# Kernel tuning notes

Measured on AMD Instinct MI355X. Metric: run time of the kernel, lower is better.

The kernel has to match this reference:

```python
import jax, jax.numpy as jnp
import numpy as np
from math import comb

N_DERIV = 4          # num_derivatives
ODE_DIM = 512        # ode_dimension
K = ODE_DIM * (N_DERIV + 1)


def _build_system(n, d):
    # system_matrices_1d: A_1d = flip(pascal), Q_1d = flip(hilbert), chol(Q_1d)
    x = np.arange(n + 1)
    B = np.array([[comb(i, j) for j in range(n + 1)] for i in range(n + 1)], dtype=np.float64)
    A1 = B[::-1, ::-1]                                  # flip both axes
    Hil = 1.0 / (x[:, None] + x[None, :] + 1.0)
    Q1 = Hil[::-1, ::-1]
    L1 = np.linalg.cholesky(Q1)
    a = np.kron(np.eye(d), A1)
    q = np.kron(np.eye(d), L1)
    return jnp.asarray(a, jnp.float32), jnp.asarray(q, jnp.float32)


def _qr_r(x):
    # sqrtm_to_cholesky: upper-triangular factor from reduced QR
    return jnp.linalg.qr(x)[1]


def setup_inputs() -> dict:
    key = jax.random.key(0)
    k1, k2, k3, k4, k5 = jax.random.split(key, 5)
    a, q_sqrtm_lower = _build_system(N_DERIV, ODE_DIM)
    m0 = jax.random.normal(k1, (K,), dtype=jnp.float32)
    l0 = jnp.tril(jax.random.normal(k2, (K, K), dtype=jnp.float32) * 0.05)
    H = jax.random.normal(k3, (ODE_DIM, K), dtype=jnp.float32) * 0.1
    bias = jax.random.normal(k4, (ODE_DIM,), dtype=jnp.float32)
    dt = jax.random.uniform(k5, (1,), dtype=jnp.float32, minval=0.05, maxval=0.15)
    return {"m0": m0, "l0": l0, "H": H, "bias": bias, "dt": dt,
            "a": a, "q_sqrtm_lower": q_sqrtm_lower}


def reference(m0, l0, H, bias, dt, a, q_sqrtm_lower):
    d = H.shape[0]
    k = m0.shape[0]
    n1 = k // d                       # num_derivatives + 1
    # --- assemble_preconditioner ---
    powers = jnp.arange(n1 - 1, -1, -1, dtype=m0.dtype)
    scales = jnp.exp(jax.lax.lgamma(powers + 1.0))
    pw = powers + 0.5
    adt = jnp.abs(dt[0])
    p = jnp.tile(adt ** pw / scales, d)          # (k,)
    p_inv = jnp.tile(adt ** (-pw) * scales, d)   # (k,)
    # --- extrapolate_mean ---
    m0_p = p_inv * m0
    m_ext_p = a @ m0_p
    m_ext = p * m_ext_p
    # EK-style linearized observation residual
    m_obs = H @ m_ext - bias                     # (d,)
    # --- estimate_error ---
    l_obs_ns_e = H @ (p_inv[:, None] * q_sqrtm_lower)            # (d,k)
    l_obs_raw = _qr_r(l_obs_ns_e.T).T                            # lower (d,d)
    res_white = jax.scipy.linalg.solve_triangular(l_obs_raw.T, m_obs, lower=False)
    diffusion = jnp.sqrt(jnp.dot(res_white, res_white) / res_white.size)
    error = diffusion * jnp.sqrt(jnp.einsum('nj,nj->n', l_obs_raw, l_obs_raw))
    # --- complete_extrapolation (sum_of_sqrtm_factors) ---
    R1 = (a @ (p_inv[:, None] * l0)).T           # (k,k)
    R2 = (diffusion * q_sqrtm_lower).T           # (k,k)
    l_ext_p = _qr_r(jnp.vstack([R1, R2])).T      # lower (k,k)
    l_ext = p[:, None] * l_ext_p
    # --- final_correction ---
    l_obs_ns = H @ l_ext                         # (d,k)
    l_obs = _qr_r(l_obs_ns.T).T                  # lower (d,d)
    crosscov = l_ext @ l_obs_ns.T                # (k,d)
    gain = jax.scipy.linalg.cho_solve((l_obs, True), crosscov.T).T  # (k,d)
    m_cor = m_ext - gain @ m_obs
    l_cor = l_ext - gain @ l_obs_ns
    u = jnp.reshape(m_cor, (-1, d), order='F')[0]  # derivative-0 block
    return m_cor, l_cor, u, error, diffusion
```

## Files before the change

### kernel.cpp

```cpp
#include <hip/hip_runtime.h>
#include <math.h>

#define KDIM 2560
#define DDIM 512
#define NB 64

#define QM 2560
#define QM2 1024
#define QN 512
#define PW 16
#define UW 4

#define OUT_LCOR 2560
#define OUT_U    6556160
#define OUT_ERR  6556672
#define OUT_DIFF 6557184


__global__ void k_setup(const float* dt, double* scal){
  if (threadIdx.x==0 && blockIdx.x==0){
    double adt = fabs((double)dt[0]);
    const double scales[5] = {24.0,6.0,2.0,1.0,1.0};
    for (int i=0;i<5;i++){
      double pw = (double)(4-i)+0.5;
      scal[i]   = pow(adt, pw)/scales[i];
      scal[5+i] = pow(adt,-pw)*scales[i];
    }
  }
}

__global__ __launch_bounds__(256) void k_mext_mobs(const float* a, const float* m0, const float* H,
                                                   const float* bias, const double* scal,
                                                   double* mext, double* mobs){
  __shared__ double me[KDIM];
  __shared__ double red[256];
  double pp[5], pv[5];
  #pragma unroll
  for (int i=0;i<5;i++){ pp[i]=scal[i]; pv[i]=scal[5+i]; }
  int tid=threadIdx.x;
  for (int r=tid; r<KDIM; r+=256){
    int j=r/5, i=r%5;
    const float* arow = a + (size_t)r*KDIM + 5*j;
    const float* m0b  = m0 + 5*j;
    double acc=0;
    #pragma unroll
    for (int l=0;l<5;l++) acc += (double)arow[l]*pv[l]*(double)m0b[l];
    me[r] = pp[i]*acc;
  }
  __syncthreads();
  if (blockIdx.x==0) for (int r=tid;r<KDIM;r+=256) mext[r]=me[r];
  int b = blockIdx.x;
  const float* Hr = H + (size_t)b*KDIM;
  double acc=0;
  for (int c=tid;c<KDIM;c+=256) acc += (double)Hr[c]*me[c];
  red[tid]=acc; __syncthreads();
  for (int s=128;s>0;s>>=1){ if (tid<s) red[tid]+=red[tid+s]; __syncthreads(); }
  if (tid==0) mobs[b] = red[0] - (double)bias[b];
}

__global__ void k_A2(const float* H, const float* q, const double* scal,
                     double* Atop, double* Abot){
  int idx = blockIdx.x*blockDim.x+threadIdx.x;
  if (idx >= QN*QM) return;
  double pv[5];
  #pragma unroll
  for (int t=0;t<5;t++) pv[t]=scal[5+t];
  int j = idx / QM;
  int i = idx % QM;
  int bi = i/5;
  double acc=0;
  #pragma unroll
  for (int t=0;t<5;t++)
    acc += (double)H[(size_t)j*QM + 5*bi+t]*pv[t]*(double)q[(size_t)(5*bi+t)*QM + i];
  if (i < 512) Atop[(size_t)j*QM2 + i] = acc;
  else         Abot[(size_t)j*2048 + (i-512)] = acc;
}

__global__ void k_copyB(const double* Gbot, double* AQ){
  int idx = blockIdx.x*blockDim.x+threadIdx.x;
  if (idx >= 512*512) return;
  int c = idx/512, rr = idx%512;
  AQ[(size_t)c*QM2 + 512 + rr] = (rr<=c) ? Gbot[(size_t)c*512 + rr] : 0.0;
}

__global__ __launch_bounds__(1024) void qr_panel(double* A, double* vhead, int col0, double* Tbuf){
  __shared__ double redw[16][PW];
  __shared__ double rednorm[16];
  __shared__ double sh[3];
  __shared__ double wsh[PW];
  __shared__ double alphas[PW], betas[PW];
  __shared__ double VtVs[PW][PW];
  __shared__ double Tsh[PW][PW];
  int tid=threadIdx.x, wid=tid>>6, lane=tid&63;
  int m = QM2 - col0;
  bool on = tid < m;
  double x[PW];
  #pragma unroll
  for (int j=0;j<PW;j++)
    x[j] = on ? A[(size_t)(col0+j)*QM2 + col0 + tid] : 0.0;
  for (int j=0;j<PW;j++){
    double v0 = (tid>=j && on)? x[j] : 0.0;
    double ps = v0*v0;
    #pragma unroll
    for (int o=32;o>0;o>>=1) ps += __shfl_down(ps,o);
    if (lane==0) rednorm[wid]=ps;
    if (tid==j) sh[0]=x[j];
    __syncthreads();
    if (tid==0){
      double s0=0;
      for (int t=0;t<16;t++) s0+=rednorm[t];
      double x1=sh[0];
      double nrm=sqrt(s0);
      double alpha=(x1>=0.0)?-nrm:nrm;
      double v1=x1-alpha;
      double vtv=s0-2.0*alpha*x1+alpha*alpha;
      double b=(vtv>0.0)?2.0/vtv:0.0;
      sh[1]=v1; sh[2]=b;
      alphas[j]=alpha; betas[j]=b;
      vhead[col0+j]=v1;
    }
    __syncthreads();
    if (tid==j) x[j]=sh[1];
    double b=sh[2];
    double v=(tid>=j && on)? x[j] : 0.0;
    #pragma unroll
    for (int t=0;t<PW;t++){
      if (t==j) continue;
      double p=v*x[t];
      #pragma unroll
      for (int o=32;o>0;o>>=1) p+=__shfl_down(p,o);
      if (lane==0) redw[wid][t]=p;
    }
    __syncthreads();
    if (tid<PW && tid!=j){
      double tot=0;
      #pragma unroll
      for (int t2=0;t2<16;t2++) tot+=redw[t2][tid];
      if (tid>j) wsh[tid]=b*tot;
      else       VtVs[tid][j]=tot;
    }
    __syncthreads();
    if (v!=0.0){
      for (int t=j+1;t<PW;t++) x[t]-=wsh[t]*v;
    }
  }
  __syncthreads();
  if (tid<PW){
    int i=tid;
    Tsh[i][i]=betas[i];
    for (int j2=i+1;j2<PW;j2++){
      double z=0;
      for (int t=i;t<j2;t++) z+=Tsh[i][t]*VtVs[t][j2];
      Tsh[i][j2]=-betas[j2]*z;
    }
  }
  __syncthreads();
  for (int e=tid;e<PW*PW;e+=1024){
    int i=e/PW, j2=e%PW;
    Tbuf[e] = (j2>=i)? Tsh[i][j2] : 0.0;
  }
  if (on){
    #pragma unroll
    for (int j=0;j<PW;j++)
      A[(size_t)(col0+j)*QM2 + col0 + tid] = (tid==j)? alphas[j] : x[j];
  }
}

__global__ __launch_bounds__(256) void qr_update(double* A, const double* vhead,
                                                 const double* Tbuf, int col0){
  __shared__ double redu[4][PW];
  __shared__ double ysh[PW];
  __shared__ double wsh[PW];
  int tid=threadIdx.x, wid=tid>>6, lane=tid&63;
  int cc=col0+PW+blockIdx.x;
  int m=QM2-col0;
  double a[UW];
  #pragma unroll
  for (int w=0;w<UW;w++){
    int lr=tid+w*256;
    a[w]=(lr<m)? A[(size_t)cc*QM2+col0+lr] : 0.0;
  }
  double acc[PW];
  #pragma unroll
  for (int j=0;j<PW;j++) acc[j]=0;
  #pragma unroll
  for (int w=0;w<UW;w++){
    int lr=tid+w*256;
    if (lr<m){
      #pragma unroll
      for (int j=0;j<PW;j++){
        double vj;
        if (lr>j)       vj=A[(size_t)(col0+j)*QM2+col0+lr];
        else if (lr==j) vj=vhead[col0+j];
        else            vj=0.0;
        acc[j]+=vj*a[w];
      }
    }
  }
  #pragma unroll
  for (int j=0;j<PW;j++){
    double d=acc[j];
    #pragma unroll
    for (int o=32;o>0;o>>=1) d+=__shfl_down(d,o);
    if (lane==0) redu[wid][j]=d;
  }
  __syncthreads();
  if (tid<PW){
    double y=0;
    #pragma unroll
    for (int t=0;t<4;t++) y+=redu[t][tid];
    ysh[tid]=y;
  }
  __syncthreads();
  if (tid<PW){
    double s=0;
    for (int t=0;t<=tid;t++) s+=Tbuf[t*PW+tid]*ysh[t];
    wsh[tid]=s;
  }
  __syncthreads();
  #pragma unroll
  for (int w=0;w<UW;w++){
    int lr=tid+w*256;
    if (lr<m){
      double s=0;
      #pragma unroll
      for (int j=0;j<PW;j++){
        double vj;
        if (lr>j)       vj=A[(size_t)(col0+j)*QM2+col0+lr];
        else if (lr==j) vj=vhead[col0+j];
        else            vj=0.0;
        s+=vj*wsh[j];
      }
      A[(size_t)cc*QM2+col0+lr]=a[w]-s;
    }
  }
}

__global__ __launch_bounds__(512) void k_rpost(const double* Aq, const double* mobs,
                                               double* scal, float* out){
  __shared__ double b[DDIM];
  __shared__ double xs[DDIM];
  __shared__ double D[NB][NB+1];
  __shared__ double red[DDIM];
  __shared__ double g1sh[DDIM];
  int tid=threadIdx.x;
  {
    double s=0;
    for (int r=0;r<=tid;r++){ double v=Aq[(size_t)tid*QM2 + r]; s+=v*v; }
    g1sh[tid]=s;
  }
  b[tid]=mobs[tid];
  __syncthreads();
  for (int p=7;p>=0;p--){
    int b0=p*NB;
    for (int e=tid;e<NB*NB;e+=512){ int i=e&63, j2=e>>6; D[i][j2]=Aq[(size_t)(b0+j2)*QM2 + b0+i]; }
    __syncthreads();
    if (tid<64){
      double bi=b[b0+tid];
      for (int k=NB-1;k>=0;k--){
        double bk=__shfl(bi,k);
        double xk=bk/D[k][k];
        if (tid<k) bi-=D[tid][k]*xk;
        if (tid==k) bi=xk;
      }
      xs[b0+tid]=bi;
    }
    __syncthreads();
    if (tid<b0){
      double s=0;
      #pragma unroll 8
      for (int j2=0;j2<NB;j2++) s+=Aq[(size_t)(b0+j2)*QM2 + tid]*xs[b0+j2];
      b[tid]-=s;
    }
    __syncthreads();
  }
  red[tid]=xs[tid]*xs[tid]; __syncthreads();
  for (int s=256;s>0;s>>=1){ if (tid<s) red[tid]+=red[tid+s]; __syncthreads(); }
  double diff=sqrt(red[0]/(double)DDIM);
  if (tid==0){ scal[10]=diff; out[OUT_DIFF]=(float)diff; }
  out[OUT_ERR+tid]=(float)(diff*sqrt(fmax(g1sh[tid],0.0)));
}

__global__ void k_X(const float* a, const float* l0, const double* scal, float* X){
  int idx=blockIdx.x*blockDim.x+threadIdx.x;
  if (idx>=KDIM*KDIM) return;
  double pv[5];
  #pragma unroll
  for (int t=0;t<5;t++) pv[t]=scal[5+t];
  int r=idx/KDIM, c=idx%KDIM;
  int j=r/5;
  const float* arow = a + (size_t)r*KDIM + 5*j;
  double acc=0;
  #pragma unroll
  for (int l=0;l<5;l++)
    acc += (double)arow[l]*pv[l]*(double)l0[(size_t)(5*j+l)*KDIM+c];
  X[idx]=(float)acc;
}

template<typename TA,int ATR,typename TB,int BTR,int MODE>
__global__ __launch_bounds__(256) void gemm64(const TA* __restrict__ A,int lda,
                                              const TB* __restrict__ B,int ldb,
                                              void* __restrict__ Cv,int ldc,
                                              int K,int kmode){
  __shared__ double As[16][65];
  __shared__ double Bs[16][65];
  int tid=threadIdx.x, tx=tid&15, ty=tid>>4;
  int n0=blockIdx.x*64, m0=blockIdx.y*64;
  int ks=0, ke=K;
  if (kmode==1) ks=n0;
  else if (kmode==2) ke=min(K,n0+64);
  else if (kmode==3) ke=min(K,m0+64);
  else if (kmode==4) ks=m0;
  double acc[4][4]={};
  for (int k0=ks;k0<ke;k0+=16){
    if (ATR){
      for (int e=tid;e<16*64;e+=256){int k=e>>6,mm=e&63; As[k][mm]=(double)A[(size_t)(k0+k)*lda+m0+mm];}
    } else {
      for (int e=tid;e<64*16;e+=256){int mm=e>>4,k=e&15; As[k][mm]=(double)A[(size_t)(m0+mm)*lda+k0+k];}
    }
    if (BTR){
      for (int e=tid;e<64*16;e+=256){int nn=e>>4,k=e&15; Bs[k][nn]=(double)B[(size_t)(n0+nn)*ldb+k0+k];}
    } else {
      for (int e=tid;e<16*64;e+=256){int k=e>>6,nn=e&63; Bs[k][nn]=(double)B[(size_t)(k0+k)*ldb+n0+nn];}
    }
    __syncthreads();
    #pragma unroll
    for (int t=0;t<16;t++){
      double av[4],bv[4];
      #pragma unroll
      for (int i=0;i<4;i++){av[i]=As[t][ty+16*i];bv[i]=Bs[t][tx+16*i];}
      #pragma unroll
      for (int i=0;i<4;i++)
        #pragma unroll
        for (int j=0;j<4;j++) acc[i][j]+=av[i]*bv[j];
    }
    __syncthreads();
  }
  #pragma unroll
  for (int i=0;i<4;i++){
    #pragma unroll
    for (int j=0;j<4;j++){
      size_t idx=(size_t)(m0+ty+16*i)*ldc+n0+tx+16*j;
      if (MODE==0) ((double*)Cv)[idx]=acc[i][j];
      else if (MODE==1) ((double*)Cv)[idx]-=acc[i][j];
      else ((float*)Cv)[idx]=(float)acc[i][j];
    }
  }
}

__global__ __launch_bounds__(256) void syrk_lower(const float* __restrict__ X, const float* __restrict__ q,
                                                  const double* __restrict__ scal,
                                                  double* __restrict__ G, int n){
  int S0=blockIdx.x*64, R0=blockIdx.y*64;
  if (S0>R0) return;
  __shared__ double As[16][65];
  __shared__ double Bs[16][65];
  int tid=threadIdx.x, tx=tid&15, ty=tid>>4;
  int kend=min(n, S0+80);
  double acc[4][4]={};
  for (int k0=0;k0<kend;k0+=16){
    for (int e=tid;e<64*16;e+=256){int mm=e>>4,k=e&15; As[k][mm]=(double)X[(size_t)(R0+mm)*n+k0+k];}
    for (int e=tid;e<64*16;e+=256){int nn=e>>4,k=e&15; Bs[k][nn]=(double)X[(size_t)(S0+nn)*n+k0+k];}
    __syncthreads();
    #pragma unroll
    for (int t=0;t<16;t++){
      double av[4],bv[4];
      #pragma unroll
      for (int i=0;i<4;i++){av[i]=As[t][ty+16*i];bv[i]=Bs[t][tx+16*i];}
      #pragma unroll
      for (int i=0;i<4;i++)
        #pragma unroll
        for (int j=0;j<4;j++) acc[i][j]+=av[i]*bv[j];
    }
    __syncthreads();
  }
  double dd = scal[10]*scal[10];
  #pragma unroll
  for (int i=0;i<4;i++)
    #pragma unroll
    for (int j=0;j<4;j++){
      int r=R0+ty+16*i, c=S0+tx+16*j;
      double v=acc[i][j];
      if (c<=r && (r/5)==(c/5)){
        double qq=0;
        #pragma unroll
        for (int k=0;k<5;k++) qq += (double)q[(size_t)(r%5)*KDIM+k]*(double)q[(size_t)(c%5)*KDIM+k];
        v += dd*qq;
      }
      G[(size_t)r*n+c]=v;
    }
}

__global__ __launch_bounds__(256) void chol_diag(double* A, int n, int k0){
  __shared__ double P[NB][NB+1];
  int tid=threadIdx.x;
  for (int e=tid;e<NB*NB;e+=256){int r=e>>6,c=e&63;P[r][c]=A[(size_t)(k0+r)*n+k0+c];}
  int tx=tid&15, ty=tid>>4;
  __syncthreads();
  for (int j=0;j<NB;j++){
    double pj=P[j][j];
    __syncthreads();
    double rpj=1.0/sqrt(fmax(pj,1e-280));
    if (tid>j && tid<NB) P[tid][j]*=rpj;
    if (tid==j) P[j][j]=sqrt(fmax(pj,1e-280));
    __syncthreads();
    #pragma unroll
    for (int a2=0;a2<4;a2++){
      int r=ty+16*a2;
      double lrj=P[r][j];
      #pragma unroll
      for (int b2=0;b2<4;b2++){
        int c=tx+16*b2;
        if (r>j && c>j && c<=r) P[r][c]-=lrj*P[c][j];
      }
    }
    __syncthreads();
  }
  for (int e=tid;e<NB*NB;e+=256){int r=e>>6,c=e&63;A[(size_t)(k0+r)*n+k0+c]=P[r][c];}
}

__global__ __launch_bounds__(256) void chol_trsm(double* A,int n,int k0){
  __shared__ double Ls[NB][NB+1];
  __shared__ double St[NB][NB+1];
  __shared__ double rec[NB];
  int tid=threadIdx.x;
  for (int e=tid;e<NB*NB;e+=256){int r=e>>6,c=e&63;Ls[r][c]=A[(size_t)(k0+r)*n+k0+c];}
  __syncthreads();
  if (tid<NB) rec[tid]=1.0/Ls[tid][tid];
  int base=k0+NB+blockIdx.x*256;
  int myrow=base+tid;
  int mychunk=tid>>6, lrow=tid&63;
  double ar[NB];
  for (int ch=0;ch<4;ch++){
    int r0=base+ch*64;
    for (int e=tid;e<NB*NB;e+=256){
      int r=e>>6,c=e&63;
      if (r0+r<n) St[r][c]=A[(size_t)(r0+r)*n+k0+c];
    }
    __syncthreads();
    if (mychunk==ch && myrow<n){
      #pragma unroll
      for (int c=0;c<NB;c++) ar[c]=St[lrow][c];
    }
    __syncthreads();
  }
  if (myrow<n){
    #pragma unroll
    for (int j=0;j<NB;j++){
      double s=ar[j];
      #pragma unroll
      for (int t=0;t<j;t++) s-=ar[t]*Ls[j][t];
      ar[j]=s*rec[j];
    }
  }
  for (int ch=0;ch<4;ch++){
    int r0=base+ch*64;
    if (mychunk==ch && myrow<n){
      #pragma unroll
      for (int c=0;c<NB;c++) St[lrow][c]=ar[c];
    }
    __syncthreads();
    for (int e=tid;e<NB*NB;e+=256){
      int r=e>>6,c=e&63;
      if (r0+r<n) A[(size_t)(r0+r)*n+k0+c]=St[r][c];
    }
    __syncthreads();
  }
}

__global__ __launch_bounds__(256) void chol_syrk_fd(double* A,int n,int k0){
  int ts0=k0+NB;
  int S0=ts0+blockIdx.x*64, R0=ts0+blockIdx.y*64;
  if (S0>R0) return;
  __shared__ double As[16][65];
  __shared__ double Bs[16][65];
  __shared__ double P[NB][NB+1];
  int tid=threadIdx.x, tx=tid&15, ty=tid>>4;
  double acc[4][4]={};
  for (int k0i=0;k0i<NB;k0i+=16){
    for (int e=tid;e<64*16;e+=256){int mm=e>>4,k=e&15; As[k][mm]=A[(size_t)(R0+mm)*n+k0+k0i+k];}
    for (int e=tid;e<64*16;e+=256){int nn=e>>4,k=e&15; Bs[k][nn]=A[(size_t)(S0+nn)*n+k0+k0i+k];}
    __syncthreads();
    #pragma unroll
    for (int t=0;t<16;t++){
      double av[4],bv[4];
      #pragma unroll
      for (int i=0;i<4;i++){av[i]=As[t][ty+16*i];bv[i]=Bs[t][tx+16*i];}
      #pragma unroll
      for (int i=0;i<4;i++)
        #pragma unroll
        for (int j=0;j<4;j++) acc[i][j]+=av[i]*bv[j];
    }
    __syncthreads();
  }
  if (!(blockIdx.x==0 && blockIdx.y==0)){
    #pragma unroll
    for (int i=0;i<4;i++)
      #pragma unroll
      for (int j=0;j<4;j++)
        A[(size_t)(R0+ty+16*i)*n+S0+tx+16*j]-=acc[i][j];
    return;
  }
  #pragma unroll
  for (int i=0;i<4;i++)
    #pragma unroll
    for (int j=0;j<4;j++)
      P[ty+16*i][tx+16*j] = A[(size_t)(R0+ty+16*i)*n+S0+tx+16*j] - acc[i][j];
  __syncthreads();
  for (int j=0;j<NB;j++){
    double pj=P[j][j];
    __syncthreads();
    double rpj=1.0/sqrt(fmax(pj,1e-280));
    if (tid>j && tid<NB) P[tid][j]*=rpj;
    if (tid==j) P[j][j]=sqrt(fmax(pj,1e-280));
    __syncthreads();
    #pragma unroll
    for (int a2=0;a2<4;a2++){
      int r=ty+16*a2;
      double lrj=P[r][j];
      #pragma unroll
      for (int b2=0;b2<4;b2++){
        int c=tx+16*b2;
        if (r>j && c>j && c<=r) P[r][c]-=lrj*P[c][j];
      }
    }
    __syncthreads();
  }
  for (int e=tid;e<NB*NB;e+=256){int r=e>>6,c=e&63;A[(size_t)(ts0+r)*n+ts0+c]=P[r][c];}
}

__global__ void k_extract(const double* G2, const double* scal, float* lext){
  int idx=blockIdx.x*blockDim.x+threadIdx.x;
  if (idx>=KDIM*KDIM) return;
  int r=idx/KDIM, c=idx%KDIM;
  double v = (c<=r)? scal[r%5]*G2[idx] : 0.0;
  lext[idx]=(float)v;
}

__global__ __launch_bounds__(256) void trinv_diag(const double* S, double* Linv){
  __shared__ double Ls[NB][NB+1];
  __shared__ double Ti[NB][NB+1];
  int jb=blockIdx.x, tid=threadIdx.x;
  for (int e=tid; e<DDIM*NB; e+=256){
    int r=e/NB, c=e%NB;
    Linv[(size_t)r*DDIM + jb*NB + c]=0.0;
  }
  for (int e=tid;e<NB*NB;e+=256){int r=e>>6,c=e&63; Ls[r][c]=S[(size_t)(jb*NB+r)*DDIM + jb*NB+c];}
  __syncthreads();
  if (tid<NB){
    int c=tid;
    for (int r=c;r<NB;r++){
      double s=(r==c)?1.0:0.0;
      for (int t=c;t<r;t++) s-=Ls[r][t]*Ti[t][c];
      Ti[r][c]=s/Ls[r][r];
    }
    for (int r=0;r<c;r++) Ti[r][c]=0.0;
  }
  __syncthreads();
  for (int e=tid;e<NB*NB;e+=256){int r=e>>6,c=e&63; Linv[(size_t)(jb*NB+r)*DDIM + jb*NB+c]=Ti[r][c];}
}

__global__ __launch_bounds__(256) void trinv_step(const double* S, double* Linv, int d){
  __shared__ double As[16][65];
  __shared__ double Bs[16][65];
  __shared__ double Ps[NB][NB+1];
  int jb=blockIdx.x, ib=jb+d;
  int tid=threadIdx.x, tx=tid&15, ty=tid>>4;
  double acc[4][4]={};
  int kstart=jb*NB, kend=ib*NB;
  for (int k0=kstart;k0<kend;k0+=16){
    for (int e=tid;e<64*16;e+=256){int mm=e>>4,k=e&15; As[k][mm]=S[(size_t)(ib*NB+mm)*DDIM + k0+k];}
    for (int e=tid;e<16*64;e+=256){int k=e>>6,nn=e&63; Bs[k][nn]=Linv[(size_t)(k0+k)*DDIM + jb*NB+nn];}
    __syncthreads();
    #pragma unroll
    for (int t=0;t<16;t++){
      double av[4],bv[4];
      #pragma unroll
      for (int i=0;i<4;i++){av[i]=As[t][ty+16*i];bv[i]=Bs[t][tx+16*i];}
      #pragma unroll
      for (int i=0;i<4;i++)
        #pragma unroll
        for (int j=0;j<4;j++) acc[i][j]+=av[i]*bv[j];
    }
    __syncthreads();
  }
  #pragma unroll
  for (int i=0;i<4;i++)
    #pragma unroll
    for (int j=0;j<4;j++) Ps[ty+16*i][tx+16*j]=acc[i][j];
  double o[4][4]={};
  __syncthreads();
  for (int k0=0;k0<NB;k0+=16){
    for (int e=tid;e<64*16;e+=256){int mm=e>>4,k=e&15; As[k][mm]=Linv[(size_t)(ib*NB+mm)*DDIM + ib*NB+k0+k];}
    __syncthreads();
    #pragma unroll
    for (int t=0;t<16;t++){
      double av[4],bv[4];
      #pragma unroll
      for (int i=0;i<4;i++){av[i]=As[t][ty+16*i];bv[i]=Ps[k0+t][tx+16*i];}
      #pragma unroll
      for (int i=0;i<4;i++)
        #pragma unroll
        for (int j=0;j<4;j++) o[i][j]+=av[i]*bv[j];
    }
    __syncthreads();
  }
  #pragma unroll
  for (int i=0;i<4;i++)
    #pragma unroll
    for (int j=0;j<4;j++)
      Linv[(size_t)(ib*NB+ty+16*i)*DDIM + jb*NB+tx+16*j] = -o[i][j];
}

__global__ void k_mcor(const double* Z, const double* mobs, const double* mext, float* out){
  __shared__ double mo[DDIM];
  for (int s=threadIdx.x;s<DDIM;s+=256) mo[s]=mobs[s];
  __syncthreads();
  int r=blockIdx.x*256+threadIdx.x;
  if (r>=KDIM) return;
  double acc=0;
  for (int s=0;s<DDIM;s++) acc += Z[(size_t)s*KDIM+r]*mo[s];
  double mc = mext[r]-acc;
  out[r]=(float)mc;
  if (r%5==0) out[OUT_U + r/5]=(float)mc;
}

__global__ __launch_bounds__(256) void k_lcor(const double* __restrict__ Z, const float* __restrict__ lobs,
                                              const float* __restrict__ lext, float* __restrict__ out){
  __shared__ double As[16][65];
  __shared__ double Bs[16][65];
  int tid=threadIdx.x, tx=tid&15, ty=tid>>4;
  int n0=blockIdx.x*64, m0=blockIdx.y*64;
  double acc[4][4]={};
  for (int k0=0;k0<DDIM;k0+=16){
    for (int e=tid;e<16*64;e+=256){int k=e>>6,mm=e&63; As[k][mm]=Z[(size_t)(k0+k)*KDIM+m0+mm];}
    for (int e=tid;e<16*64;e+=256){int k=e>>6,nn=e&63; Bs[k][nn]=(double)lobs[(size_t)(k0+k)*KDIM+n0+nn];}
    __syncthreads();
    #pragma unroll
    for (int t=0;t<16;t++){
      double av[4],bv[4];
      #pragma unroll
      for (int i=0;i<4;i++){av[i]=As[t][ty+16*i];bv[i]=Bs[t][tx+16*i];}
      #pragma unroll
      for (int i=0;i<4;i++)
        #pragma unroll
        for (int j=0;j<4;j++) acc[i][j]+=av[i]*bv[j];
    }
    __syncthreads();
  }
  #pragma unroll
  for (int i=0;i<4;i++)
    #pragma unroll
    for (int j=0;j<4;j++){
      size_t idx=(size_t)(m0+ty+16*i)*KDIM+n0+tx+16*j;
      out[OUT_LCOR+idx]=(float)((double)lext[idx]-acc[i][j]);
    }
}

extern "C" void kernel_launch(void* const* d_in, const int* in_sizes, int n_in,
                              void* d_out, int out_size, void* d_ws, size_t ws_size,
                              hipStream_t stream) {
  const float* m0  = (const float*)d_in[0];
  const float* l0  = (const float*)d_in[1];
  const float* H   = (const float*)d_in[2];
  const float* bias= (const float*)d_in[3];
  const float* dt  = (const float*)d_in[4];
  const float* a   = (const float*)d_in[5];
  const float* q   = (const float*)d_in[6];
  float* out = (float*)d_out;

  char* w=(char*)d_ws;
  auto alloc=[&](size_t bytes)->char*{ char* p=w; w += ((bytes+255)/256)*256; return p; };
  double* scal  =(double*)alloc(16*8);
  double* mext  =(double*)alloc((size_t)KDIM*8);
  double* mobs  =(double*)alloc((size_t)DDIM*8);
  double* vheadA=(double*)alloc((size_t)QN*8);
  double* Tbuf  =(double*)alloc((size_t)PW*PW*8);
  double* AQ    =(double*)alloc((size_t)QM2*QN*8);
  double* S     =(double*)alloc((size_t)DDIM*DDIM*8);
  double* G2    =(double*)alloc((size_t)KDIM*KDIM*8);
  float*  LOBS  =(float*) alloc((size_t)DDIM*KDIM*4);
  float*  X     =(float*) alloc((size_t)KDIM*KDIM*4);
  float*  LEXT  = X;
  double* Abot  = G2;
  double* Gbot  = Abot + (size_t)2048*512;
  double* Linv  = G2;
  double* C2    = Linv + (size_t)DDIM*DDIM;
  double* Y     = C2   + (size_t)DDIM*KDIM;
  double* Z     = Y    + (size_t)DDIM*KDIM;

  k_setup<<<1,1,0,stream>>>(dt, scal);
  k_mext_mobs<<<DDIM,256,0,stream>>>(a, m0, H, bias, scal, mext, mobs);

  k_A2<<<(QN*QM+255)/256,256,0,stream>>>(H, q, scal, AQ, Abot);
  gemm64<double,0,double,1,0><<<dim3(8,8),256,0,stream>>>(Abot,2048, Abot,2048, Gbot,512, 2048, 0);
  chol_diag<<<1,256,0,stream>>>(Gbot,512,0);
  for (int k0=0;k0+NB<512;k0+=NB){
    int m = 512-k0-NB;
    chol_trsm<<<(m+255)/256,256,0,stream>>>(Gbot,512,k0);
    chol_syrk_fd<<<dim3(m/64,m/64),256,0,stream>>>(Gbot,512,k0);
  }
  k_copyB<<<(512*512+255)/256,256,0,stream>>>(Gbot, AQ);
  for (int p=0;p<QN/PW;p++){
    int col0=p*PW;
    qr_panel<<<1,1024,0,stream>>>(AQ, vheadA, col0, Tbuf);
    int ntr = QN - col0 - PW;
    if (ntr>0) qr_update<<<ntr,256,0,stream>>>(AQ, vheadA, Tbuf, col0);
  }
  k_rpost<<<1,512,0,stream>>>(AQ, mobs, scal, out);

  k_X<<<(KDIM*KDIM+255)/256,256,0,stream>>>(a, l0, scal, X);
  syrk_lower<<<dim3(KDIM/64,KDIM/64),256,0,stream>>>(X, q, scal, G2, KDIM);
  chol_diag<<<1,256,0,stream>>>(G2, KDIM, 0);
  for (int k0=0;k0+NB<KDIM;k0+=NB){
    int m = KDIM-k0-NB;
    chol_trsm<<<(m+255)/256,256,0,stream>>>(G2, KDIM, k0);
    chol_syrk_fd<<<dim3(m/64,m/64),256,0,stream>>>(G2, KDIM, k0);
  }
  k_extract<<<(KDIM*KDIM+255)/256,256,0,stream>>>(G2, scal, LEXT);

  gemm64<float,0,float,0,2><<<dim3(KDIM/64,DDIM/64),256,0,stream>>>(H,KDIM, LEXT,KDIM, LOBS,KDIM, KDIM, 1);
  gemm64<float,0,float,1,0><<<dim3(DDIM/64,DDIM/64),256,0,stream>>>(LOBS,KDIM, LOBS,KDIM, S,DDIM, KDIM, 0);
  chol_diag<<<1,256,0,stream>>>(S, DDIM, 0);
  for (int k0=0;k0+NB<DDIM;k0+=NB){
    int m = DDIM-k0-NB;
    chol_trsm<<<(m+255)/256,256,0,stream>>>(S, DDIM, k0);
    chol_syrk_fd<<<dim3(m/64,m/64),256,0,stream>>>(S, DDIM, k0);
  }
  trinv_diag<<<8,256,0,stream>>>(S, Linv);
  for (int d=1;d<8;d++)
    trinv_step<<<8-d,256,0,stream>>>(S, Linv, d);
  gemm64<float,0,float,1,0><<<dim3(KDIM/64,DDIM/64),256,0,stream>>>(LOBS,KDIM, LEXT,KDIM, C2,KDIM, KDIM, 2);
  gemm64<double,0,double,0,0><<<dim3(KDIM/64,DDIM/64),256,0,stream>>>(Linv,DDIM, C2,KDIM, Y,KDIM, DDIM, 3);
  gemm64<double,1,double,0,0><<<dim3(KDIM/64,DDIM/64),256,0,stream>>>(Linv,DDIM, Y,KDIM, Z,KDIM, DDIM, 4);

  k_mcor<<<(KDIM+255)/256,256,0,stream>>>(Z, mobs, mext, out);
  k_lcor<<<dim3(KDIM/64,KDIM/64),256,0,stream>>>(Z, LOBS, LEXT, out);
}
```

Measured before the change: 15.90 ms.

## Fuse blocked Cholesky into one cooperative kernel; trim QR rows and SYRK grid

Replaces the per-step launch sequence of Cholesky diagonal/trsm/syrk kernels with a single cooperative persistent kernel that uses grid.sync between stages, folding the next diagonal factorization into the trailing update. This removes many small launches and their serialization overhead. The QR panel and update now process only the first 528 rows, on the premise that rows below that are zero in the stacked triangular input, so the panel needs fewer threads. The SYRK launch now maps a 1D grid onto lower-triangular tiles, so no blocks are launched only to exit. A cooperative launch falling back to the old path adds risk, and grid-wide syncs may cost more than launches if occupancy limits residency.

```diff
diff --git a/kernel.cpp b/kernel.cpp
--- a/kernel.cpp
+++ b/kernel.cpp
@@ -1,5 +1,8 @@
 #include <hip/hip_runtime.h>
+#include <hip/hip_cooperative_groups.h>
 #include <math.h>
+
+namespace cg = cooperative_groups;
 
 #define KDIM 2560
 #define DDIM 512
@@ -9,7 +12,8 @@
 #define QM2 1024
 #define QN 512
 #define PW 16
-#define UW 4
+#define UW 3
+#define QACT 528
 
 #define OUT_LCOR 2560
 #define OUT_U    6556160
@@ -83,16 +87,16 @@
   AQ[(size_t)c*QM2 + 512 + rr] = (rr<=c) ? Gbot[(size_t)c*512 + rr] : 0.0;
 }
 
-__global__ __launch_bounds__(1024) void qr_panel(double* A, double* vhead, int col0, double* Tbuf){
-  __shared__ double redw[16][PW];
-  __shared__ double rednorm[16];
+__global__ __launch_bounds__(576) void qr_panel(double* A, double* vhead, int col0, double* Tbuf){
+  __shared__ double redw[9][PW];
+  __shared__ double rednorm[9];
   __shared__ double sh[3];
   __shared__ double wsh[PW];
   __shared__ double alphas[PW], betas[PW];
   __shared__ double VtVs[PW][PW];
   __shared__ double Tsh[PW][PW];
   int tid=threadIdx.x, wid=tid>>6, lane=tid&63;
-  int m = QM2 - col0;
+  int m = QM2 - col0; if (m > QACT) m = QACT;
   bool on = tid < m;
   double x[PW];
   #pragma unroll
@@ -108,7 +112,7 @@
     __syncthreads();
     if (tid==0){
       double s0=0;
-      for (int t=0;t<16;t++) s0+=rednorm[t];
+      for (int t=0;t<9;t++) s0+=rednorm[t];
       double x1=sh[0];
       double nrm=sqrt(s0);
       double alpha=(x1>=0.0)?-nrm:nrm;
@@ -135,7 +139,7 @@
     if (tid<PW && tid!=j){
       double tot=0;
       #pragma unroll
-      for (int t2=0;t2<16;t2++) tot+=redw[t2][tid];
+      for (int t2=0;t2<9;t2++) tot+=redw[t2][tid];
       if (tid>j) wsh[tid]=b*tot;
       else       VtVs[tid][j]=tot;
     }
@@ -155,7 +159,7 @@
     }
   }
   __syncthreads();
-  for (int e=tid;e<PW*PW;e+=1024){
+  for (int e=tid;e<PW*PW;e+=576){
     int i=e/PW, j2=e%PW;
     Tbuf[e] = (j2>=i)? Tsh[i][j2] : 0.0;
   }
@@ -173,7 +177,7 @@
   __shared__ double wsh[PW];
   int tid=threadIdx.x, wid=tid>>6, lane=tid&63;
   int cc=col0+PW+blockIdx.x;
-  int m=QM2-col0;
+  int m=QM2-col0; if (m > QACT) m = QACT;
   double a[UW];
   #pragma unroll
   for (int w=0;w<UW;w++){
@@ -351,8 +355,13 @@
 __global__ __launch_bounds__(256) void syrk_lower(const float* __restrict__ X, const float* __restrict__ q,
                                                   const double* __restrict__ scal,
                                                   double* __restrict__ G, int n){
-  int S0=blockIdx.x*64, R0=blockIdx.y*64;
-  if (S0>R0) return;
+  int t = blockIdx.x;
+  int u = (int)((sqrtf(8.0f*(float)t+1.0f)+1.0f)*0.5f);
+  while ((u*(u-1))/2 > t) u--;
+  while ((u*(u+1))/2 <= t) u++;
+  int s = (KDIM/64) - u;
+  int r = s + (t - (u*(u-1))/2);
+  int S0=s*64, R0=r*64;
   __shared__ double As[16][65];
   __shared__ double Bs[16][65];
   int tid=threadIdx.x, tx=tid&15, ty=tid>>4;
@@ -363,10 +372,10 @@
     for (int e=tid;e<64*16;e+=256){int nn=e>>4,k=e&15; Bs[k][nn]=(double)X[(size_t)(S0+nn)*n+k0+k];}
     __syncthreads();
     #pragma unroll
-    for (int t=0;t<16;t++){
+    for (int t2=0;t2<16;t2++){
       double av[4],bv[4];
       #pragma unroll
-      for (int i=0;i<4;i++){av[i]=As[t][ty+16*i];bv[i]=Bs[t][tx+16*i];}
+      for (int i=0;i<4;i++){av[i]=As[t2][ty+16*i];bv[i]=Bs[t2][tx+16*i];}
       #pragma unroll
       for (int i=0;i<4;i++)
         #pragma unroll
@@ -379,15 +388,15 @@
   for (int i=0;i<4;i++)
     #pragma unroll
     for (int j=0;j<4;j++){
-      int r=R0+ty+16*i, c=S0+tx+16*j;
+      int rr=R0+ty+16*i, c=S0+tx+16*j;
       double v=acc[i][j];
-      if (c<=r && (r/5)==(c/5)){
+      if (c<=rr && (rr/5)==(c/5)){
         double qq=0;
         #pragma unroll
-        for (int k=0;k<5;k++) qq += (double)q[(size_t)(r%5)*KDIM+k]*(double)q[(size_t)(c%5)*KDIM+k];
+        for (int k=0;k<5;k++) qq += (double)q[(size_t)(rr%5)*KDIM+k]*(double)q[(size_t)(c%5)*KDIM+k];
         v += dd*qq;
       }
-      G[(size_t)r*n+c]=v;
+      G[(size_t)rr*n+c]=v;
     }
 }
 
@@ -527,6 +536,143 @@
     __syncthreads();
   }
   for (int e=tid;e<NB*NB;e+=256){int r=e>>6,c=e&63;A[(size_t)(ts0+r)*n+ts0+c]=P[r][c];}
+}
+
+__device__ __forceinline__ void fact64(double (*P)[NB+1], int tid, int tx, int ty){
+  for (int j=0;j<NB;j++){
+    double pj=P[j][j];
+    __syncthreads();
+    double rpj=1.0/sqrt(fmax(pj,1e-280));
+    if (tid>j && tid<NB) P[tid][j]*=rpj;
+    if (tid==j) P[j][j]=sqrt(fmax(pj,1e-280));
+    __syncthreads();
+    #pragma unroll
+    for (int a2=0;a2<4;a2++){
+      int r=ty+16*a2;
+      double lrj=P[r][j];
+      #pragma unroll
+      for (int b2=0;b2<4;b2++){
+        int c=tx+16*b2;
+        if (r>j && c>j && c<=r) P[r][c]-=lrj*P[c][j];
+      }
+    }
+    __syncthreads();
+  }
+}
+
+__global__ __launch_bounds__(256,2) void chol_coop(double* __restrict__ A, int n){
+  cg::grid_group grid = cg::this_grid();
+  __shared__ double sm[64*65 + 64 + 32*65];
+  double (*Ls)[NB+1] = (double(*)[NB+1])sm;
+  double* rec        = sm + 64*65;
+  double (*St)[NB+1] = (double(*)[NB+1])(sm + 64*65 + 64);
+  double (*As)[NB+1] = (double(*)[NB+1])sm;
+  double (*Bs)[NB+1] = (double(*)[NB+1])(sm + 16*65);
+  double (*P)[NB+1]  = (double(*)[NB+1])(sm + 32*65);
+  int tid=threadIdx.x, tx=tid&15, ty=tid>>4;
+
+  if (blockIdx.x==0){
+    for (int e=tid;e<NB*NB;e+=256){int r=e>>6,c=e&63;P[r][c]=A[(size_t)r*n+c];}
+    __syncthreads();
+    fact64(P, tid, tx, ty);
+    for (int e=tid;e<NB*NB;e+=256){int r=e>>6,c=e&63;A[(size_t)r*n+c]=P[r][c];}
+  }
+  grid.sync();
+
+  for (int k0=0;k0+NB<n;k0+=NB){
+    int m=n-k0-NB;
+    int nch=(m+255)/256;
+    for (int c0=blockIdx.x;c0<nch;c0+=gridDim.x){
+      int base=k0+NB+c0*256;
+      __syncthreads();
+      for (int e=tid;e<NB*NB;e+=256){int r=e>>6,cc=e&63;Ls[r][cc]=A[(size_t)(k0+r)*n+k0+cc];}
+      __syncthreads();
+      if (tid<NB) rec[tid]=1.0/Ls[tid][tid];
+      int myrow=base+tid, mychunk=tid>>5, lrow=tid&31;
+      double ar[NB];
+      for (int ch=0;ch<8;ch++){
+        int r0=base+ch*32;
+        for (int e=tid;e<32*NB;e+=256){
+          int r=e>>6,cc=e&63;
+          if (r0+r<n) St[r][cc]=A[(size_t)(r0+r)*n+k0+cc];
+        }
+        __syncthreads();
+        if (mychunk==ch && myrow<n){
+          #pragma unroll
+          for (int cc=0;cc<NB;cc++) ar[cc]=St[lrow][cc];
+        }
+        __syncthreads();
+      }
+      if (myrow<n){
+        #pragma unroll
+        for (int j=0;j<NB;j++){
+          double s=ar[j];
+          #pragma unroll
+          for (int t2=0;t2<j;t2++) s-=ar[t2]*Ls[j][t2];
+          ar[j]=s*rec[j];
+        }
+      }
+      for (int ch=0;ch<8;ch++){
+        int r0=base+ch*32;
+        if (mychunk==ch && myrow<n){
+          #pragma unroll
+          for (int cc=0;cc<NB;cc++) St[lrow][cc]=ar[cc];
+        }
+        __syncthreads();
+        for (int e=tid;e<32*NB;e+=256){
+          int r=e>>6,cc=e&63;
+          if (r0+r<n) A[(size_t)(r0+r)*n+k0+cc]=St[r][cc];
+        }
+        __syncthreads();
+      }
+    }
+    grid.sync();
+    int T=m/64;
+    int ntile=T*(T+1)/2;
+    int ts0=k0+NB;
+    for (int t=blockIdx.x;t<ntile;t+=gridDim.x){
+      int r=(int)((sqrtf(8.0f*(float)t+1.0f)-1.0f)*0.5f);
+      while ((r*(r+1))/2 > t) r--;
+      while (((r+1)*(r+2))/2 <= t) r++;
+      int s=t-(r*(r+1))/2;
+      int R0=ts0+r*64, S0=ts0+s*64;
+      __syncthreads();
+      double acc[4][4]={};
+      for (int k0i=0;k0i<NB;k0i+=16){
+        for (int e=tid;e<64*16;e+=256){int mm=e>>4,k=e&15; As[k][mm]=A[(size_t)(R0+mm)*n+k0+k0i+k];}
+        for (int e=tid;e<64*16;e+=256){int nn=e>>4,k=e&15; Bs[k][nn]=A[(size_t)(S0+nn)*n+k0+k0i+k];}
+        __syncthreads();
+        #pragma unroll
+        for (int tt=0;tt<16;tt++){
+          double av[4],bv[4];
+          #pragma unroll
+          for (int i=0;i<4;i++){av[i]=As[tt][ty+16*i];bv[i]=Bs[tt][tx+16*i];}
+          #pragma unroll
+          for (int i=0;i<4;i++)
+            #pragma unroll
+            for (int j=0;j<4;j++) acc[i][j]+=av[i]*bv[j];
+        }
+        __syncthreads();
+      }
+      if (t!=0){
+        #pragma unroll
+        for (int i=0;i<4;i++)
+          #pragma unroll
+          for (int j=0;j<4;j++)
+            A[(size_t)(R0+ty+16*i)*n+S0+tx+16*j]-=acc[i][j];
+      } else {
+        #pragma unroll
+        for (int i=0;i<4;i++)
+          #pragma unroll
+          for (int j=0;j<4;j++)
+            P[ty+16*i][tx+16*j]=A[(size_t)(R0+ty+16*i)*n+S0+tx+16*j]-acc[i][j];
+        __syncthreads();
+        fact64(P, tid, tx, ty);
+        for (int e=tid;e<NB*NB;e+=256){int r2=e>>6,c2=e&63;A[(size_t)(ts0+r2)*n+ts0+c2]=P[r2][c2];}
+      }
+    }
+    grid.sync();
+  }
 }
 
 __global__ void k_extract(const double* G2, const double* scal, float* lext){
@@ -689,44 +835,44 @@
   double* Y     = C2   + (size_t)DDIM*KDIM;
   double* Z     = Y    + (size_t)DDIM*KDIM;
 
+  auto chol_full=[&](double* M, int n, int nblk){
+    double* Mp=M; int nn=n;
+    void* args[2] = { (void*)&Mp, (void*)&nn };
+    hipError_t ce = hipLaunchCooperativeKernel((const void*)chol_coop, dim3(nblk), dim3(256),
+                                               args, 0, stream);
+    if (ce != hipSuccess){
+      chol_diag<<<1,256,0,stream>>>(M, n, 0);
+      for (int k0=0;k0+NB<n;k0+=NB){
+        int m = n-k0-NB;
+        chol_trsm<<<(m+255)/256,256,0,stream>>>(M,n,k0);
+        chol_syrk_fd<<<dim3(m/64,m/64),256,0,stream>>>(M,n,k0);
+      }
+    }
+  };
+
   k_setup<<<1,1,0,stream>>>(dt, scal);
   k_mext_mobs<<<DDIM,256,0,stream>>>(a, m0, H, bias, scal, mext, mobs);
 
   k_A2<<<(QN*QM+255)/256,256,0,stream>>>(H, q, scal, AQ, Abot);
   gemm64<double,0,double,1,0><<<dim3(8,8),256,0,stream>>>(Abot,2048, Abot,2048, Gbot,512, 2048, 0);
-  chol_diag<<<1,256,0,stream>>>(Gbot,512,0);
-  for (int k0=0;k0+NB<512;k0+=NB){
-    int m = 512-k0-NB;
-    chol_trsm<<<(m+255)/256,256,0,stream>>>(Gbot,512,k0);
-    chol_syrk_fd<<<dim3(m/64,m/64),256,0,stream>>>(Gbot,512,k0);
-  }
+  chol_full(Gbot, 512, 64);
   k_copyB<<<(512*512+255)/256,256,0,stream>>>(Gbot, AQ);
   for (int p=0;p<QN/PW;p++){
     int col0=p*PW;
-    qr_panel<<<1,1024,0,stream>>>(AQ, vheadA, col0, Tbuf);
+    qr_panel<<<1,576,0,stream>>>(AQ, vheadA, col0, Tbuf);
     int ntr = QN - col0 - PW;
     if (ntr>0) qr_update<<<ntr,256,0,stream>>>(AQ, vheadA, Tbuf, col0);
   }
   k_rpost<<<1,512,0,stream>>>(AQ, mobs, scal, out);
 
   k_X<<<(KDIM*KDIM+255)/256,256,0,stream>>>(a, l0, scal, X);
-  syrk_lower<<<dim3(KDIM/64,KDIM/64),256,0,stream>>>(X, q, scal, G2, KDIM);
-  chol_diag<<<1,256,0,stream>>>(G2, KDIM, 0);
-  for (int k0=0;k0+NB<KDIM;k0+=NB){
-    int m = KDIM-k0-NB;
-    chol_trsm<<<(m+255)/256,256,0,stream>>>(G2, KDIM, k0);
-    chol_syrk_fd<<<dim3(m/64,m/64),256,0,stream>>>(G2, KDIM, k0);
-  }
+  syrk_lower<<<(KDIM/64)*((KDIM/64)+1)/2,256,0,stream>>>(X, q, scal, G2, KDIM);
+  chol_full(G2, KDIM, 512);
   k_extract<<<(KDIM*KDIM+255)/256,256,0,stream>>>(G2, scal, LEXT);
 
   gemm64<float,0,float,0,2><<<dim3(KDIM/64,DDIM/64),256,0,stream>>>(H,KDIM, LEXT,KDIM, LOBS,KDIM, KDIM, 1);
   gemm64<float,0,float,1,0><<<dim3(DDIM/64,DDIM/64),256,0,stream>>>(LOBS,KDIM, LOBS,KDIM, S,DDIM, KDIM, 0);
-  chol_diag<<<1,256,0,stream>>>(S, DDIM, 0);
-  for (int k0=0;k0+NB<DDIM;k0+=NB){
-    int m = DDIM-k0-NB;
-    chol_trsm<<<(m+255)/256,256,0,stream>>>(S, DDIM, k0);
-    chol_syrk_fd<<<dim3(m/64,m/64),256,0,stream>>>(S, DDIM, k0);
-  }
+  chol_full(S, DDIM, 64);
   trinv_diag<<<8,256,0,stream>>>(S, Linv);
   for (int d=1;d<8;d++)
     trinv_step<<<8-d,256,0,stream>>>(S, Linv, d);
```

Result: slower. 18.15 ms (+14.2%).
